# Optimization experiments

Hardware: AMD Instinct MI355X
Metric: run time of the kernel (lower is better)

## Reference

```python
import jax, jax.numpy as jnp
import numpy as np


def _update_cv(features, labels, ave, cov, amount, class_num):
    # Segment-reduce formulation of the onehot-expand update_CV.
    N, A = features.shape
    C = class_num
    counts = jax.ops.segment_sum(jnp.ones((N,), features.dtype), labels, num_segments=C)  # [C]
    sums = jax.ops.segment_sum(features, labels, num_segments=C)  # [C, A]
    denom = jnp.where(counts == 0, 1.0, counts)[:, None]  # Amount_CxA with zeros -> 1
    ave_CxA = sums / denom
    # var_temp: sum over samples of (x - mean_label)^2, divided by count
    diff = features - ave_CxA[labels]  # [N, A]
    sq = jax.ops.segment_sum(diff * diff, labels, num_segments=C)
    var_temp = sq / denom
    sum_weight = counts[:, None]  # [C,1] broadcast over A
    weight_CV = sum_weight / (sum_weight + amount[:, None])
    weight_CV = jnp.nan_to_num(weight_CV, nan=0.0)
    additional_CV = weight_CV * (1 - weight_CV) * (ave - ave_CxA) ** 2
    new_cov = cov * (1 - weight_CV) + var_temp * weight_CV + additional_CV
    new_ave = ave * (1 - weight_CV) + ave_CxA * weight_CV
    new_amount = amount + counts
    return new_ave, new_cov, new_amount


def _isda_aug(fc_weight, y, labels, cv_matrix, ratio):
    # sigma2[n,c] = ratio * sum_a (W[c,a] - W[labels[n],a])^2 * CV[labels[n],a]
    # = ratio * ( (W^2) @ cv_n - 2 W @ (w_n * cv_n) + sum_a w_n^2 cv_n )
    cv_n = cv_matrix[labels]              # [N, A]
    w_n = fc_weight[labels]               # [N, A]
    t1 = cv_n @ (fc_weight ** 2).T        # [N, C]
    t2 = (w_n * cv_n) @ fc_weight.T       # [N, C]
    t3 = jnp.sum(w_n * w_n * cv_n, axis=1, keepdims=True)  # [N, 1]
    sigma2 = ratio * (t1 - 2.0 * t2 + t3)
    return y + 0.5 * sigma2


def setup_inputs() -> dict:
    key = jax.random.key(0)
    k1, k2, k3, k4 = jax.random.split(key, 4)
    N, A, C = 512, 2048, 1000
    features = jax.random.normal(k1, (N, A), dtype=jnp.float32)
    labels = jax.random.randint(k2, (N,), 0, C)
    fc_weight = jax.random.normal(k3, (C, A), dtype=jnp.float32) * 0.02
    fc_bias = jax.random.normal(k4, (C,), dtype=jnp.float32) * 0.02
    return {
        "features": features,
        "labels": labels,
        "fc_weight": fc_weight,
        "fc_bias": fc_bias,
        "ave_state": jnp.zeros((C, A), jnp.float32),
        "cov_state": jnp.zeros((C, A), jnp.float32),
        "amount_state": jnp.zeros((C,), jnp.float32),
        "ratio": 1,
    }


def reference(features, labels, fc_weight, fc_bias, ave_state, cov_state, amount_state, ratio):
    C = fc_weight.shape[0]
    # model head: y = features @ W^T + b (features come from backbone; detached for CV)
    y = features @ fc_weight.T + fc_bias
    new_ave, new_cov, new_amount = _update_cv(
        jax.lax.stop_gradient(features), labels, ave_state, cov_state, amount_state, C)
    isda_y = _isda_aug(fc_weight, y, labels, jax.lax.stop_gradient(new_cov), ratio)
    log_probs = jax.nn.log_softmax(isda_y, axis=1)
    loss = -jnp.mean(jnp.take_along_axis(log_probs, labels[:, None], axis=1))
    return loss, y, new_ave, new_cov, new_amount
```

## Files before the change

kernel.cpp:

```cpp
#include <hip/hip_runtime.h>
#include <hip/hip_bf16.h>

typedef short v8s __attribute__((ext_vector_type(8)));
typedef float v4f __attribute__((ext_vector_type(4)));

#define KSPLIT 4

static __device__ __forceinline__ float ldv(const void* p, size_t i, int f32m) {
    if (f32m) return ((const float*)p)[i];
    return __bfloat162float(((const __hip_bfloat16*)p)[i]);
}
static __device__ __forceinline__ void stv(void* p, size_t i, float v, int f32m) {
    if (f32m) ((float*)p)[i] = v;
    else ((__hip_bfloat16*)p)[i] = __float2bfloat16(v);
}
static __device__ __forceinline__ unsigned short f2bu(float x) {
    __hip_bfloat16 h = __float2bfloat16(x);
    return *(unsigned short*)&h;
}
static __device__ __forceinline__ float bu2f(unsigned short u) {
    return __uint_as_float(((unsigned)u) << 16);
}
static __device__ __forceinline__ void ld2(const void* p, size_t i, int f32m, float* o) {
    if (f32m) {
        float2 v = *(const float2*)((const float*)p + i);
        o[0] = v.x; o[1] = v.y;
    } else {
        unsigned u = *(const unsigned*)((const unsigned short*)p + i);
        o[0] = bu2f((unsigned short)(u & 0xffffu));
        o[1] = bu2f((unsigned short)(u >> 16));
    }
}

static __device__ __forceinline__ float decode_scalar(const void* p) {
    unsigned u = *(const unsigned*)p;
    unsigned e32 = (u >> 23) & 0xff;
    if (e32 >= 97 && e32 <= 160) return __uint_as_float(u);
    unsigned lo = u & 0xffffu;
    unsigned e16 = (lo >> 7) & 0xff;
    if ((u >> 16) == 0 && e16 >= 97 && e16 <= 160)
        return __uint_as_float(lo << 16);
    return (float)(int)u;
}

static __device__ __forceinline__ int block_sniff(const void* feat) {
    const __hip_bfloat16* p = (const __hip_bfloat16*)feat;
    float v = __bfloat162float(p[threadIdx.x & 255]);
    int bad = !(fabsf(v) < 1e10f);
    return __syncthreads_or(bad) ? 1 : 0;
}

__device__ __forceinline__ float wave_sum(float v) {
    #pragma unroll
    for (int o = 32; o > 0; o >>= 1) v += __shfl_down(v, o, 64);
    return v;
}
__device__ __forceinline__ float wave_max(float v) {
    #pragma unroll
    for (int o = 32; o > 0; o >>= 1) v = fmaxf(v, __shfl_down(v, o, 64));
    return v;
}

static __device__ __forceinline__ void ld16(unsigned short* lds, const unsigned short* g) {
    __builtin_amdgcn_global_load_lds(
        (const __attribute__((address_space(1))) unsigned int*)g,
        (__attribute__((address_space(3))) unsigned int*)lds,
        16, 0, 0);
}

__global__ __launch_bounds__(1024) void sort_prep(
        const int* __restrict__ labels, int* __restrict__ counts,
        int* __restrict__ offs, int* __restrict__ rows, int Nn, int C,
        const void* __restrict__ feat, unsigned short* __restrict__ featb, int total,
        float* __restrict__ lsum, int* __restrict__ lcnt) {
    __shared__ int h[1024];
    __shared__ int o[1024];
    __shared__ int cu[1024];
    int tid = threadIdx.x;
    if (blockIdx.x == 0) {
        h[tid] = 0;
        __syncthreads();
        for (int i = tid; i < Nn; i += 1024) atomicAdd(&h[labels[i]], 1);
        __syncthreads();
        o[tid] = h[tid];
        __syncthreads();
        for (int d = 1; d < 1024; d <<= 1) {
            int v = (tid >= d) ? o[tid - d] : 0;
            __syncthreads();
            o[tid] += v;
            __syncthreads();
        }
        int excl = o[tid] - h[tid];
        counts[tid] = h[tid];
        offs[tid] = excl;
        cu[tid] = excl;
        __syncthreads();
        for (int i = tid; i < Nn; i += 1024) {
            int pos = atomicAdd(&cu[labels[i]], 1);
            rows[pos] = i;
        }
        if (tid == 0) { *lsum = 0.f; *lcnt = 0; }
    } else {
        int f32m = block_sniff(feat);
        int i = ((blockIdx.x - 1) * 1024 + tid) * 8;
        if (i >= total) return;
        if (f32m) {
            const float* f = (const float*)feat + i;
            unsigned short r[8];
            #pragma unroll
            for (int u = 0; u < 8; ++u) r[u] = f2bu(f[u]);
            *(v8s*)(featb + i) = *(v8s*)r;
        } else {
            *(v8s*)(featb + i) = *(const v8s*)((const unsigned short*)feat + i);
        }
    }
}

__global__ __launch_bounds__(256) void finalize_stats(
        const unsigned short* __restrict__ featb,
        const int* __restrict__ counts, const int* __restrict__ offs,
        const int* __restrict__ rows,
        const void* __restrict__ ave, const void* __restrict__ cov,
        const void* __restrict__ amount, const void* __restrict__ W,
        const void* __restrict__ feat,
        void* __restrict__ out, size_t off_ave, size_t off_cov, size_t off_amt,
        unsigned short* __restrict__ Wb, unsigned short* __restrict__ W2b,
        unsigned short* __restrict__ Cb, unsigned short* __restrict__ Gb,
        float* __restrict__ T3p, int A, int A8) {
    __shared__ float sb[4];
    int f32m = block_sniff(feat);
    int c = blockIdx.y;
    int a = (blockIdx.x * 256 + threadIdx.x) * 2;
    size_t idx = (size_t)c * A + a;
    int cnti = counts[c];
    int start = offs[c];
    float s1[2] = {0.f, 0.f}, s2[2] = {0.f, 0.f};
    for (int i = 0; i < cnti; ++i) {
        unsigned u = *(const unsigned*)(featb + (size_t)rows[start + i] * A + a);
        float x0 = bu2f((unsigned short)(u & 0xffffu));
        float x1 = bu2f((unsigned short)(u >> 16));
        s1[0] += x0; s2[0] += x0 * x0;
        s1[1] += x1; s2[1] += x1 * x1;
    }
    float cnt = (float)cnti;
    float denom = cnti > 0 ? cnt : 1.f;
    float amt = ldv(amount, c, f32m);
    float tot = cnt + amt;
    float w = tot > 0.f ? (cnt / tot) : 0.f;
    float av[2], cv[2], wv[2];
    ld2(ave, idx, f32m, av);
    ld2(cov, idx, f32m, cv);
    ld2(W, idx, f32m, wv);
    unsigned short cb2[2], gb2[2];
    float t3s = 0.f;
    #pragma unroll
    for (int k = 0; k < 2; ++k) {
        float mean = s1[k] / denom;
        float var = fmaxf((s2[k] - cnt * mean * mean) / denom, 0.f);
        float d = av[k] - mean;
        float ncv = cv[k] * (1.f - w) + var * w + w * (1.f - w) * d * d;
        float nav = av[k] * (1.f - w) + mean * w;
        stv(out, off_cov + idx + k, ncv, f32m);
        stv(out, off_ave + idx + k, nav, f32m);
        cb2[k] = f2bu(ncv);
        gb2[k] = f2bu(ncv * wv[k]);
        t3s += wv[k] * wv[k] * ncv;
    }
    *(unsigned*)(Wb + idx)  = (unsigned)f2bu(wv[0]) | ((unsigned)f2bu(wv[1]) << 16);
    *(unsigned*)(W2b + idx) = (unsigned)f2bu(wv[0] * wv[0]) | ((unsigned)f2bu(wv[1] * wv[1]) << 16);
    *(unsigned*)(Cb + idx)  = (unsigned)cb2[0] | ((unsigned)cb2[1] << 16);
    *(unsigned*)(Gb + idx)  = (unsigned)gb2[0] | ((unsigned)gb2[1] << 16);
    if (a == 0) stv(out, off_amt + c, amt + cnt, f32m);
    float s = wave_sum(t3s);
    int lane = threadIdx.x & 63, wid = threadIdx.x >> 6;
    if (lane == 0) sb[wid] = s;
    __syncthreads();
    if (threadIdx.x == 0) T3p[(size_t)c * A8 + blockIdx.x] = sb[0] + sb[1] + sb[2] + sb[3];
}

__global__ __launch_bounds__(256) void triple_gemm_mfma(
        const unsigned short* __restrict__ featb,
        const unsigned short* __restrict__ Wb,
        const unsigned short* __restrict__ W2b,
        const unsigned short* __restrict__ Cb,
        const unsigned short* __restrict__ Gb,
        const int* __restrict__ labels,
        float* __restrict__ partY, float* __restrict__ partT1, float* __restrict__ partT2,
        int Cpad, int A, size_t NC) {
    __shared__ unsigned short sA[3][10240];
    __shared__ int sLab[64];
    int tid = threadIdx.x, wv = tid >> 6, lane = tid & 63;
    int n0 = blockIdx.y * 64, j0 = blockIdx.x * 64;
    int kslice = A / KSPLIT;
    int k0 = blockIdx.z * kslice;
    if (tid < 64) sLab[tid] = labels[n0 + tid];
    __syncthreads();

    int r = lane & 15, q = lane >> 4;
    int fr = wv * 16 + r;
    const unsigned short* pF = featb + (size_t)(n0 + fr) * A + k0 + q * 8;
    int lab = sLab[fr];
    const unsigned short* pC = Cb + (size_t)lab * A + k0 + q * 8;
    const unsigned short* pG = Gb + (size_t)lab * A + k0 + q * 8;
    const unsigned short* pW = Wb + (size_t)(j0 + fr) * A + k0 + q * 8;
    const unsigned short* pQ = W2b + (size_t)(j0 + fr) * A + k0 + q * 8;

    v4f aY[4] = {{0,0,0,0},{0,0,0,0},{0,0,0,0},{0,0,0,0}};
    v4f aT1[4] = {{0,0,0,0},{0,0,0,0},{0,0,0,0},{0,0,0,0}};
    v4f aT2[4] = {{0,0,0,0},{0,0,0,0},{0,0,0,0},{0,0,0,0}};

    const int NIT = kslice / 32;

    #define STAGE(b) do { \
        ld16(&sA[b][0    + wv * 512], pF); \
        ld16(&sA[b][2048 + wv * 512], pC); \
        ld16(&sA[b][4096 + wv * 512], pG); \
        ld16(&sA[b][6144 + wv * 512], pW); \
        ld16(&sA[b][8192 + wv * 512], pQ); \
        pF += 32; pC += 32; pG += 32; pW += 32; pQ += 32; } while (0)

    STAGE(0);
    STAGE(1);

    for (int it = 0; it < NIT; ++it) {
        int bcur = it % 3;
        if (it + 1 < NIT) asm volatile("s_waitcnt vmcnt(5)\n\ts_barrier" ::: "memory");
        else              asm volatile("s_waitcnt vmcnt(0)\n\ts_barrier" ::: "memory");
        if (it + 2 < NIT) { int bn = (it + 2) % 3; STAGE(bn); }
        v8s f = *(v8s*)&sA[bcur][0    + wv * 512 + lane * 8];
        v8s c = *(v8s*)&sA[bcur][2048 + wv * 512 + lane * 8];
        v8s g = *(v8s*)&sA[bcur][4096 + wv * 512 + lane * 8];
        #pragma unroll
        for (int t = 0; t < 4; ++t) {
            v8s w  = *(v8s*)&sA[bcur][6144 + t * 512 + lane * 8];
            v8s w2 = *(v8s*)&sA[bcur][8192 + t * 512 + lane * 8];
            aY[t]  = __builtin_amdgcn_mfma_f32_16x16x32_bf16(f, w,  aY[t],  0, 0, 0);
            aT1[t] = __builtin_amdgcn_mfma_f32_16x16x32_bf16(c, w2, aT1[t], 0, 0, 0);
            aT2[t] = __builtin_amdgcn_mfma_f32_16x16x32_bf16(g, w,  aT2[t], 0, 0, 0);
        }
    }
    #undef STAGE

    float* pY = partY + (size_t)blockIdx.z * NC;
    float* p1 = partT1 + (size_t)blockIdx.z * NC;
    float* p2 = partT2 + (size_t)blockIdx.z * NC;
    int quad = lane >> 4, colb = lane & 15;
    #pragma unroll
    for (int t = 0; t < 4; ++t) {
        int j = j0 + t * 16 + colb;
        #pragma unroll
        for (int rr = 0; rr < 4; ++rr) {
            int n = n0 + wv * 16 + quad * 4 + rr;
            size_t idx = (size_t)n * Cpad + j;
            pY[idx] = aY[t][rr];
            p1[idx] = aT1[t][rr];
            p2[idx] = aT2[t][rr];
        }
    }
}

__global__ __launch_bounds__(256) void epilogue_rowloss(
        const float* __restrict__ partY, const float* __restrict__ partT1,
        const float* __restrict__ partT2, const float* __restrict__ T3p,
        const void* __restrict__ bias, const void* __restrict__ feat,
        const int* __restrict__ labels,
        void* __restrict__ out, size_t off_y,
        float* __restrict__ lsum, int* __restrict__ lcnt,
        int C, int Cpad, int A8, const void* ratio_p, size_t NC, int Nn) {
    __shared__ float sb[4];
    __shared__ float sM;
    __shared__ float sLabVal;
    int f32m = block_sniff(feat);
    int tid = threadIdx.x;
    int n = blockIdx.x;
    int lab = labels[n];
    float t3 = 0.f;
    for (int i = 0; i < A8; ++i) t3 += T3p[(size_t)lab * A8 + i];
    float ratio = decode_scalar(ratio_p);

    float vals[8];
    int nu = Cpad >> 8;
    float m = -3.4e38f;
    for (int u = 0; u < nu; ++u) {
        int j = u * 256 + tid;
        float v = -3.4e38f;
        if (j < C) {
            size_t idx = (size_t)n * Cpad + j;
            float y = 0.f, t1 = 0.f, t2 = 0.f;
            #pragma unroll
            for (int z = 0; z < KSPLIT; ++z) {
                y  += partY[z * NC + idx];
                t1 += partT1[z * NC + idx];
                t2 += partT2[z * NC + idx];
            }
            y += ldv(bias, j, f32m);
            stv(out, off_y + (size_t)n * C + j, y, f32m);
            v = y + 0.5f * ratio * (t1 - 2.f * t2 + t3);
            if (j == lab) sLabVal = v;
        }
        vals[u] = v;
        m = fmaxf(m, v);
    }
    m = wave_max(m);
    int lane = tid & 63, wid = tid >> 6;
    if (lane == 0) sb[wid] = m;
    __syncthreads();
    if (tid == 0) sM = fmaxf(fmaxf(sb[0], sb[1]), fmaxf(sb[2], sb[3]));
    __syncthreads();
    m = sM;
    float s = 0.f;
    for (int u = 0; u < nu; ++u) s += expf(vals[u] - m);
    __syncthreads();
    s = wave_sum(s);
    if (lane == 0) sb[wid] = s;
    __syncthreads();
    if (tid == 0) {
        float rl = m + logf(sb[0] + sb[1] + sb[2] + sb[3]) - sLabVal;
        atomicAdd(lsum, rl);
        __threadfence();
        int old = atomicAdd(lcnt, 1);
        if (old == Nn - 1) {
            __threadfence();
            float total = atomicAdd(lsum, 0.f);
            stv(out, 0, total / (float)Nn, f32m);
        }
    }
}

extern "C" void kernel_launch(void* const* d_in, const int* in_sizes, int n_in,
                              void* d_out, int out_size, void* d_ws, size_t ws_size,
                              hipStream_t stream) {
    const void* feat   = d_in[0];
    const int*  labels = (const int*)d_in[1];
    const void* W      = d_in[2];
    const void* bias   = d_in[3];
    const void* ave    = d_in[4];
    const void* cov    = d_in[5];
    const void* amount = d_in[6];
    const void* ratiop = d_in[7];

    int NA = in_sizes[0];
    int Nn = in_sizes[1];
    int C  = in_sizes[3];
    int A  = NA / Nn;
    int CA = in_sizes[2];
    int Cpad = ((C + 255) / 256) * 256;
    int A8 = A / 512;
    size_t NC = (size_t)Nn * Cpad;

    size_t off_y   = 1;
    size_t off_ave = off_y + (size_t)Nn * C;
    size_t off_cov = off_ave + (size_t)CA;
    size_t off_amt = off_cov + (size_t)CA;

    char* ws = (char*)d_ws;
    int*   w_cnt  = (int*)ws;
    int*   w_off  = w_cnt + 1024;
    int*   w_rows = w_off + 1024;
    float* w_T3p  = (float*)(w_rows + 1024);
    float* w_lsum = w_T3p + 8192;
    int*   w_lcnt = (int*)(w_lsum + 1);
    float* w_partY  = w_lsum + 1024;
    float* w_partT1 = w_partY + KSPLIT * NC;
    float* w_partT2 = w_partT1 + KSPLIT * NC;
    unsigned short* w_featb = (unsigned short*)(w_partT2 + KSPLIT * NC);
    unsigned short* w_Wb    = w_featb + NA;
    unsigned short* w_W2b   = w_Wb + CA;
    unsigned short* w_Cb    = w_W2b + CA;
    unsigned short* w_Gb    = w_Cb + CA;

    int prep_blocks = NA / 8192;
    sort_prep<<<1 + prep_blocks, 1024, 0, stream>>>(
        labels, w_cnt, w_off, w_rows, Nn, C, feat, w_featb, NA, w_lsum, w_lcnt);
    dim3 g2(A / 512, C);
    finalize_stats<<<g2, 256, 0, stream>>>(w_featb, w_cnt, w_off, w_rows,
                                           ave, cov, amount, W, feat,
                                           d_out, off_ave, off_cov, off_amt,
                                           w_Wb, w_W2b, w_Cb, w_Gb, w_T3p, A, A8);
    dim3 g3(Cpad / 64, Nn / 64, KSPLIT);
    triple_gemm_mfma<<<g3, 256, 0, stream>>>(w_featb, w_Wb, w_W2b, w_Cb, w_Gb,
                                             labels, w_partY, w_partT1, w_partT2,
                                             Cpad, A, NC);
    epilogue_rowloss<<<Nn, 256, 0, stream>>>(w_partY, w_partT1, w_partT2, w_T3p,
                                             bias, feat, labels, d_out, off_y,
                                             w_lsum, w_lcnt,
                                             C, Cpad, A8, ratiop, NC, Nn);
}
```

Measured before the change: 144.1 us.

## Fuse all four stages into one cooperative persistent kernel with grid syncs

Replaces the four separate launches (sort/prep, finalize stats, triple GEMM, epilogue) with a single cooperative kernel of 512 blocks that runs each stage as a grid-strided loop separated by grid.sync barriers. The goal is to remove per-launch overhead and inter-kernel gaps. In exchange every stage is limited to 512 blocks of 256 threads, which may reduce parallelism in the stats stage (previously C×4 blocks) and in the GEMM. The 1024-thread sort is also redone with 256 threads. If the cooperative launch fails, the code falls back to the original four launches.

```diff
diff --git a/kernel.cpp b/kernel.cpp
--- a/kernel.cpp
+++ b/kernel.cpp
@@ -1,5 +1,8 @@
 #include <hip/hip_runtime.h>
 #include <hip/hip_bf16.h>
+#include <hip/hip_cooperative_groups.h>
+
+namespace cg = cooperative_groups;
 
 typedef short v8s __attribute__((ext_vector_type(8)));
 typedef float v4f __attribute__((ext_vector_type(4)));
@@ -67,6 +70,271 @@
         (__attribute__((address_space(3))) unsigned int*)lds,
         16, 0, 0);
 }
+
+
+struct MegaArgs {
+    const void* feat; const int* labels; const void* W; const void* bias;
+    const void* ave; const void* cov; const void* amount; const void* ratiop;
+    void* out;
+    unsigned long long off_y, off_ave, off_cov, off_amt;
+    int* counts; int* offs; int* rowsg; float* T3p; float* lsum; int* lcnt;
+    float* partY; float* partT1; float* partT2;
+    unsigned short* featb; unsigned short* Wb; unsigned short* W2b;
+    unsigned short* Cb; unsigned short* Gb;
+    int Nn, C, A, Cpad, A8, total;
+    unsigned long long NC;
+};
+
+__global__ __launch_bounds__(256, 2) void isda_mega(MegaArgs p) {
+    __shared__ union {
+        struct { int h[1024]; int o[1024]; int cur[1024]; } s1;
+        struct { unsigned short sA[3][10240]; int sLab[64]; } s3;
+        struct { float sb[4]; float sM; float sLabVal; } s4;
+    } sh;
+
+    cg::grid_group grid = cg::this_grid();
+    int tid = threadIdx.x;
+    int lane = tid & 63, wid = tid >> 6;
+    int f32m = block_sniff(p.feat);
+
+    for (long long i = ((long long)blockIdx.x * 256 + tid) * 8; i < p.total;
+         i += (long long)gridDim.x * 2048) {
+        if (f32m) {
+            const float* f = (const float*)p.feat + i;
+            unsigned short rr[8];
+            #pragma unroll
+            for (int u2 = 0; u2 < 8; ++u2) rr[u2] = f2bu(f[u2]);
+            *(v8s*)(p.featb + i) = *(v8s*)rr;
+        } else {
+            *(v8s*)(p.featb + i) = *(const v8s*)((const unsigned short*)p.feat + i);
+        }
+    }
+    if (blockIdx.x == 0) {
+        for (int k = tid; k < 1024; k += 256) sh.s1.h[k] = 0;
+        __syncthreads();
+        for (int i = tid; i < p.Nn; i += 256) atomicAdd(&sh.s1.h[p.labels[i]], 1);
+        __syncthreads();
+        int a0 = sh.s1.h[4 * tid], a1 = sh.s1.h[4 * tid + 1];
+        int a2 = sh.s1.h[4 * tid + 2], a3 = sh.s1.h[4 * tid + 3];
+        int tsum = a0 + a1 + a2 + a3;
+        sh.s1.o[tid] = tsum;
+        __syncthreads();
+        for (int d = 1; d < 256; d <<= 1) {
+            int v = (tid >= d) ? sh.s1.o[tid - d] : 0;
+            __syncthreads();
+            sh.s1.o[tid] += v;
+            __syncthreads();
+        }
+        int texcl = sh.s1.o[tid] - tsum;
+        int e0 = texcl, e1 = e0 + a0, e2 = e1 + a1, e3 = e2 + a2;
+        p.counts[4 * tid] = a0; p.counts[4 * tid + 1] = a1;
+        p.counts[4 * tid + 2] = a2; p.counts[4 * tid + 3] = a3;
+        p.offs[4 * tid] = e0; p.offs[4 * tid + 1] = e1;
+        p.offs[4 * tid + 2] = e2; p.offs[4 * tid + 3] = e3;
+        sh.s1.cur[4 * tid] = e0; sh.s1.cur[4 * tid + 1] = e1;
+        sh.s1.cur[4 * tid + 2] = e2; sh.s1.cur[4 * tid + 3] = e3;
+        __syncthreads();
+        for (int i = tid; i < p.Nn; i += 256) {
+            int pos = atomicAdd(&sh.s1.cur[p.labels[i]], 1);
+            p.rowsg[pos] = i;
+        }
+        if (tid == 0) { *p.lsum = 0.f; *p.lcnt = 0; }
+    }
+    __threadfence();
+    grid.sync();
+
+    {
+        int NCH = p.A >> 9;
+        int units = p.C * NCH;
+        for (int u = blockIdx.x; u < units; u += gridDim.x) {
+            int chunk = u % NCH, c = u / NCH;
+            int a = (chunk * 256 + tid) * 2;
+            size_t idx = (size_t)c * p.A + a;
+            int cnti = p.counts[c];
+            int start = p.offs[c];
+            float s1v[2] = {0.f, 0.f}, s2v[2] = {0.f, 0.f};
+            for (int i = 0; i < cnti; ++i) {
+                unsigned uu = *(const unsigned*)(p.featb + (size_t)p.rowsg[start + i] * p.A + a);
+                float x0 = bu2f((unsigned short)(uu & 0xffffu));
+                float x1 = bu2f((unsigned short)(uu >> 16));
+                s1v[0] += x0; s2v[0] += x0 * x0;
+                s1v[1] += x1; s2v[1] += x1 * x1;
+            }
+            float cnt = (float)cnti;
+            float denomv = cnti > 0 ? cnt : 1.f;
+            float amt = ldv(p.amount, c, f32m);
+            float tot = cnt + amt;
+            float w = tot > 0.f ? (cnt / tot) : 0.f;
+            float av[2], cvv[2], wvv[2];
+            ld2(p.ave, idx, f32m, av);
+            ld2(p.cov, idx, f32m, cvv);
+            ld2(p.W, idx, f32m, wvv);
+            unsigned short cb2[2], gb2[2];
+            float t3s = 0.f;
+            #pragma unroll
+            for (int k = 0; k < 2; ++k) {
+                float mean = s1v[k] / denomv;
+                float var = fmaxf((s2v[k] - cnt * mean * mean) / denomv, 0.f);
+                float d = av[k] - mean;
+                float ncv = cvv[k] * (1.f - w) + var * w + w * (1.f - w) * d * d;
+                float nav = av[k] * (1.f - w) + mean * w;
+                stv(p.out, p.off_cov + idx + k, ncv, f32m);
+                stv(p.out, p.off_ave + idx + k, nav, f32m);
+                cb2[k] = f2bu(ncv);
+                gb2[k] = f2bu(ncv * wvv[k]);
+                t3s += wvv[k] * wvv[k] * ncv;
+            }
+            *(unsigned*)(p.Wb + idx)  = (unsigned)f2bu(wvv[0]) | ((unsigned)f2bu(wvv[1]) << 16);
+            *(unsigned*)(p.W2b + idx) = (unsigned)f2bu(wvv[0] * wvv[0]) | ((unsigned)f2bu(wvv[1] * wvv[1]) << 16);
+            *(unsigned*)(p.Cb + idx)  = (unsigned)cb2[0] | ((unsigned)cb2[1] << 16);
+            *(unsigned*)(p.Gb + idx)  = (unsigned)gb2[0] | ((unsigned)gb2[1] << 16);
+            if (a == 0) stv(p.out, p.off_amt + c, amt + cnt, f32m);
+            float s = wave_sum(t3s);
+            if (lane == 0) sh.s4.sb[wid] = s;
+            __syncthreads();
+            if (tid == 0)
+                p.T3p[(size_t)c * p.A8 + chunk] = sh.s4.sb[0] + sh.s4.sb[1] + sh.s4.sb[2] + sh.s4.sb[3];
+            __syncthreads();
+        }
+    }
+    __threadfence();
+    grid.sync();
+
+    {
+        int gx = p.Cpad >> 6, gy = p.Nn >> 6;
+        int vtot = gx * gy * KSPLIT;
+        int kslice = p.A / KSPLIT;
+        int NIT = kslice / 32;
+        for (int vb = blockIdx.x; vb < vtot; vb += gridDim.x) {
+            int x = vb % gx, y = (vb / gx) % gy, z = vb / (gx * gy);
+            __syncthreads();
+            if (tid < 64) sh.s3.sLab[tid] = p.labels[y * 64 + tid];
+            __syncthreads();
+            int n0 = y * 64, j0 = x * 64;
+            int k0 = z * kslice;
+            int r = lane & 15, q = lane >> 4;
+            int fr = wid * 16 + r;
+            const unsigned short* pF = p.featb + (size_t)(n0 + fr) * p.A + k0 + q * 8;
+            int lab = sh.s3.sLab[fr];
+            const unsigned short* pC = p.Cb + (size_t)lab * p.A + k0 + q * 8;
+            const unsigned short* pG = p.Gb + (size_t)lab * p.A + k0 + q * 8;
+            const unsigned short* pW = p.Wb + (size_t)(j0 + fr) * p.A + k0 + q * 8;
+            const unsigned short* pQ = p.W2b + (size_t)(j0 + fr) * p.A + k0 + q * 8;
+
+            v4f aY[4] = {{0,0,0,0},{0,0,0,0},{0,0,0,0},{0,0,0,0}};
+            v4f aT1[4] = {{0,0,0,0},{0,0,0,0},{0,0,0,0},{0,0,0,0}};
+            v4f aT2[4] = {{0,0,0,0},{0,0,0,0},{0,0,0,0},{0,0,0,0}};
+
+            #define STAGE3(b) do { \
+                ld16(&sh.s3.sA[b][0    + wid * 512], pF); \
+                ld16(&sh.s3.sA[b][2048 + wid * 512], pC); \
+                ld16(&sh.s3.sA[b][4096 + wid * 512], pG); \
+                ld16(&sh.s3.sA[b][6144 + wid * 512], pW); \
+                ld16(&sh.s3.sA[b][8192 + wid * 512], pQ); \
+                pF += 32; pC += 32; pG += 32; pW += 32; pQ += 32; } while (0)
+
+            STAGE3(0);
+            STAGE3(1);
+
+            for (int it = 0; it < NIT; ++it) {
+                int bcur = it % 3;
+                if (it + 1 < NIT) asm volatile("s_waitcnt vmcnt(5)\n\ts_barrier" ::: "memory");
+                else              asm volatile("s_waitcnt vmcnt(0)\n\ts_barrier" ::: "memory");
+                if (it + 2 < NIT) { STAGE3((it + 2) % 3); }
+                v8s f  = *(v8s*)&sh.s3.sA[bcur][0    + wid * 512 + lane * 8];
+                v8s c2 = *(v8s*)&sh.s3.sA[bcur][2048 + wid * 512 + lane * 8];
+                v8s g2 = *(v8s*)&sh.s3.sA[bcur][4096 + wid * 512 + lane * 8];
+                #pragma unroll
+                for (int t = 0; t < 4; ++t) {
+                    v8s w  = *(v8s*)&sh.s3.sA[bcur][6144 + t * 512 + lane * 8];
+                    v8s w2 = *(v8s*)&sh.s3.sA[bcur][8192 + t * 512 + lane * 8];
+                    aY[t]  = __builtin_amdgcn_mfma_f32_16x16x32_bf16(f,  w,  aY[t],  0, 0, 0);
+                    aT1[t] = __builtin_amdgcn_mfma_f32_16x16x32_bf16(c2, w2, aT1[t], 0, 0, 0);
+                    aT2[t] = __builtin_amdgcn_mfma_f32_16x16x32_bf16(g2, w,  aT2[t], 0, 0, 0);
+                }
+            }
+            #undef STAGE3
+
+            float* pY = p.partY + (size_t)z * p.NC;
+            float* p1 = p.partT1 + (size_t)z * p.NC;
+            float* p2 = p.partT2 + (size_t)z * p.NC;
+            int quad = lane >> 4, colb = lane & 15;
+            #pragma unroll
+            for (int t = 0; t < 4; ++t) {
+                int j = j0 + t * 16 + colb;
+                #pragma unroll
+                for (int rr2 = 0; rr2 < 4; ++rr2) {
+                    int n = n0 + wid * 16 + quad * 4 + rr2;
+                    size_t idx = (size_t)n * p.Cpad + j;
+                    pY[idx] = aY[t][rr2];
+                    p1[idx] = aT1[t][rr2];
+                    p2[idx] = aT2[t][rr2];
+                }
+            }
+        }
+    }
+    __threadfence();
+    grid.sync();
+
+    {
+        float ratio = decode_scalar(p.ratiop);
+        int nu = p.Cpad >> 8;
+        for (int n = blockIdx.x; n < p.Nn; n += gridDim.x) {
+            __syncthreads();
+            int lab = p.labels[n];
+            float t3 = 0.f;
+            for (int i = 0; i < p.A8; ++i) t3 += p.T3p[(size_t)lab * p.A8 + i];
+            float vals[8];
+            float m = -3.4e38f;
+            for (int u = 0; u < nu; ++u) {
+                int j = u * 256 + tid;
+                float v = -3.4e38f;
+                if (j < p.C) {
+                    size_t idx = (size_t)n * p.Cpad + j;
+                    float y = 0.f, t1 = 0.f, t2 = 0.f;
+                    #pragma unroll
+                    for (int zz = 0; zz < KSPLIT; ++zz) {
+                        y  += p.partY[zz * p.NC + idx];
+                        t1 += p.partT1[zz * p.NC + idx];
+                        t2 += p.partT2[zz * p.NC + idx];
+                    }
+                    y += ldv(p.bias, j, f32m);
+                    stv(p.out, p.off_y + (size_t)n * p.C + j, y, f32m);
+                    v = y + 0.5f * ratio * (t1 - 2.f * t2 + t3);
+                    if (j == lab) sh.s4.sLabVal = v;
+                }
+                vals[u] = v;
+                m = fmaxf(m, v);
+            }
+            m = wave_max(m);
+            if (lane == 0) sh.s4.sb[wid] = m;
+            __syncthreads();
+            if (tid == 0) sh.s4.sM = fmaxf(fmaxf(sh.s4.sb[0], sh.s4.sb[1]),
+                                           fmaxf(sh.s4.sb[2], sh.s4.sb[3]));
+            __syncthreads();
+            m = sh.s4.sM;
+            float s = 0.f;
+            for (int u = 0; u < nu; ++u) s += expf(vals[u] - m);
+            __syncthreads();
+            s = wave_sum(s);
+            if (lane == 0) sh.s4.sb[wid] = s;
+            __syncthreads();
+            if (tid == 0) {
+                float rl = m + logf(sh.s4.sb[0] + sh.s4.sb[1] + sh.s4.sb[2] + sh.s4.sb[3])
+                           - sh.s4.sLabVal;
+                atomicAdd(p.lsum, rl);
+                __threadfence();
+                int old = atomicAdd(p.lcnt, 1);
+                if (old == p.Nn - 1) {
+                    __threadfence();
+                    float totl = atomicAdd(p.lsum, 0.f);
+                    stv(p.out, 0, totl / (float)p.Nn, f32m);
+                }
+            }
+        }
+    }
+}
+
 
 __global__ __launch_bounds__(1024) void sort_prep(
         const int* __restrict__ labels, int* __restrict__ counts,
@@ -369,6 +637,27 @@
     unsigned short* w_Cb    = w_W2b + CA;
     unsigned short* w_Gb    = w_Cb + CA;
 
+    bool coop_ok = (C <= 1024) && ((A & 511) == 0) && ((Nn & 63) == 0) &&
+                   ((Cpad & 63) == 0) && (NA % 2048 == 0);
+    if (coop_ok) {
+        MegaArgs ma;
+        ma.feat = feat; ma.labels = labels; ma.W = W; ma.bias = bias;
+        ma.ave = ave; ma.cov = cov; ma.amount = amount; ma.ratiop = ratiop;
+        ma.out = d_out;
+        ma.off_y = off_y; ma.off_ave = off_ave; ma.off_cov = off_cov; ma.off_amt = off_amt;
+        ma.counts = w_cnt; ma.offs = w_off; ma.rowsg = w_rows; ma.T3p = w_T3p;
+        ma.lsum = w_lsum; ma.lcnt = w_lcnt;
+        ma.partY = w_partY; ma.partT1 = w_partT1; ma.partT2 = w_partT2;
+        ma.featb = w_featb; ma.Wb = w_Wb; ma.W2b = w_W2b; ma.Cb = w_Cb; ma.Gb = w_Gb;
+        ma.Nn = Nn; ma.C = C; ma.A = A; ma.Cpad = Cpad; ma.A8 = A8;
+        ma.total = NA; ma.NC = NC;
+        void* kargs[] = { &ma };
+        hipError_t e = hipLaunchCooperativeKernel((void*)isda_mega, dim3(512), dim3(256),
+                                                  kargs, 0, stream);
+        if (e == hipSuccess) return;
+        (void)hipGetLastError();
+    }
+
     int prep_blocks = NA / 8192;
     sort_prep<<<1 + prep_blocks, 1024, 0, stream>>>(
         labels, w_cnt, w_off, w_rows, Nn, C, feat, w_featb, NA, w_lsum, w_lcnt);
```

Result: slower. 496.7 us (+244.6%).

## Fuse label sort into stats kernel and merge T1/T2 accumulators

Applied to the files above, without the earlier changes.

Removes the separate sort_prep kernel. Each stats block now scans the labels itself to find its class rows and also converts features to bf16 in a grid-stride loop, which saves one launch and the single-block serial histogram/scan. Folds the -2 factor into Gb so that T1 and T2 share one MFMA accumulator, halving partial-sum writes and epilogue reads. The cost is that every block redundantly scans all labels, and accumulating T1-2T2 in one register may slightly change rounding.

```diff
diff --git a/kernel.cpp b/kernel.cpp
--- a/kernel.cpp
+++ b/kernel.cpp
@@ -68,128 +68,109 @@
         16, 0, 0);
 }
 
-__global__ __launch_bounds__(1024) void sort_prep(
-        const int* __restrict__ labels, int* __restrict__ counts,
-        int* __restrict__ offs, int* __restrict__ rows, int Nn, int C,
-        const void* __restrict__ feat, unsigned short* __restrict__ featb, int total,
-        float* __restrict__ lsum, int* __restrict__ lcnt) {
-    __shared__ int h[1024];
-    __shared__ int o[1024];
-    __shared__ int cu[1024];
-    int tid = threadIdx.x;
-    if (blockIdx.x == 0) {
-        h[tid] = 0;
-        __syncthreads();
-        for (int i = tid; i < Nn; i += 1024) atomicAdd(&h[labels[i]], 1);
-        __syncthreads();
-        o[tid] = h[tid];
-        __syncthreads();
-        for (int d = 1; d < 1024; d <<= 1) {
-            int v = (tid >= d) ? o[tid - d] : 0;
-            __syncthreads();
-            o[tid] += v;
-            __syncthreads();
-        }
-        int excl = o[tid] - h[tid];
-        counts[tid] = h[tid];
-        offs[tid] = excl;
-        cu[tid] = excl;
-        __syncthreads();
-        for (int i = tid; i < Nn; i += 1024) {
-            int pos = atomicAdd(&cu[labels[i]], 1);
-            rows[pos] = i;
-        }
-        if (tid == 0) { *lsum = 0.f; *lcnt = 0; }
-    } else {
-        int f32m = block_sniff(feat);
-        int i = ((blockIdx.x - 1) * 1024 + tid) * 8;
-        if (i >= total) return;
-        if (f32m) {
-            const float* f = (const float*)feat + i;
-            unsigned short r[8];
-            #pragma unroll
-            for (int u = 0; u < 8; ++u) r[u] = f2bu(f[u]);
-            *(v8s*)(featb + i) = *(v8s*)r;
-        } else {
-            *(v8s*)(featb + i) = *(const v8s*)((const unsigned short*)feat + i);
-        }
-    }
-}
-
-__global__ __launch_bounds__(256) void finalize_stats(
-        const unsigned short* __restrict__ featb,
-        const int* __restrict__ counts, const int* __restrict__ offs,
-        const int* __restrict__ rows,
+__global__ __launch_bounds__(256) void stats_prep(
+        const void* __restrict__ feat, const int* __restrict__ labels,
         const void* __restrict__ ave, const void* __restrict__ cov,
         const void* __restrict__ amount, const void* __restrict__ W,
-        const void* __restrict__ feat,
         void* __restrict__ out, size_t off_ave, size_t off_cov, size_t off_amt,
+        unsigned short* __restrict__ featb,
         unsigned short* __restrict__ Wb, unsigned short* __restrict__ W2b,
         unsigned short* __restrict__ Cb, unsigned short* __restrict__ Gb,
-        float* __restrict__ T3p, int A, int A8) {
+        float* __restrict__ T3p, float* __restrict__ lsum, int* __restrict__ lcnt,
+        int Nn, int A, int A8, int NA) {
+    __shared__ int sRows[2048];
+    __shared__ int sCnt;
     __shared__ float sb[4];
+    int tid = threadIdx.x;
     int f32m = block_sniff(feat);
+
+    if (f32m) {
+        int flat = blockIdx.y * gridDim.x + blockIdx.x;
+        int nblk = gridDim.x * gridDim.y;
+        for (long long i = ((long long)flat * 256 + tid) * 8; i < NA;
+             i += (long long)nblk * 2048) {
+            const float* f = (const float*)feat + i;
+            unsigned short r8[8];
+            #pragma unroll
+            for (int u = 0; u < 8; ++u) r8[u] = f2bu(f[u]);
+            *(v8s*)(featb + i) = *(v8s*)r8;
+        }
+    }
+    if (blockIdx.x == 0 && blockIdx.y == 0 && tid == 0) { *lsum = 0.f; *lcnt = 0; }
+
     int c = blockIdx.y;
-    int a = (blockIdx.x * 256 + threadIdx.x) * 2;
+    int a = (blockIdx.x * 256 + tid) * 2;
     size_t idx = (size_t)c * A + a;
-    int cnti = counts[c];
-    int start = offs[c];
-    float s1[2] = {0.f, 0.f}, s2[2] = {0.f, 0.f};
-    for (int i = 0; i < cnti; ++i) {
-        unsigned u = *(const unsigned*)(featb + (size_t)rows[start + i] * A + a);
-        float x0 = bu2f((unsigned short)(u & 0xffffu));
-        float x1 = bu2f((unsigned short)(u >> 16));
-        s1[0] += x0; s2[0] += x0 * x0;
-        s1[1] += x1; s2[1] += x1 * x1;
+    float s1v[2] = {0.f, 0.f}, s2v[2] = {0.f, 0.f};
+    int cnti = 0;
+    for (int base = 0; base < Nn; base += 2048) {
+        int lim = min(Nn - base, 2048);
+        if (tid == 0) sCnt = 0;
+        __syncthreads();
+        for (int i = tid; i < lim; i += 256)
+            if (labels[base + i] == c) { int pp = atomicAdd(&sCnt, 1); sRows[pp] = base + i; }
+        __syncthreads();
+        int cl = sCnt;
+        cnti += cl;
+        for (int i = 0; i < cl; ++i) {
+            float x[2];
+            ld2(feat, (size_t)sRows[i] * A + a, f32m, x);
+            s1v[0] += x[0]; s2v[0] += x[0] * x[0];
+            s1v[1] += x[1]; s2v[1] += x[1] * x[1];
+        }
+        __syncthreads();
     }
     float cnt = (float)cnti;
-    float denom = cnti > 0 ? cnt : 1.f;
+    float denomv = cnti > 0 ? cnt : 1.f;
     float amt = ldv(amount, c, f32m);
     float tot = cnt + amt;
     float w = tot > 0.f ? (cnt / tot) : 0.f;
-    float av[2], cv[2], wv[2];
+    float av[2], cvv[2], wvv[2];
     ld2(ave, idx, f32m, av);
-    ld2(cov, idx, f32m, cv);
-    ld2(W, idx, f32m, wv);
+    ld2(cov, idx, f32m, cvv);
+    ld2(W, idx, f32m, wvv);
     unsigned short cb2[2], gb2[2];
     float t3s = 0.f;
     #pragma unroll
     for (int k = 0; k < 2; ++k) {
-        float mean = s1[k] / denom;
-        float var = fmaxf((s2[k] - cnt * mean * mean) / denom, 0.f);
+        float mean = s1v[k] / denomv;
+        float var = fmaxf((s2v[k] - cnt * mean * mean) / denomv, 0.f);
         float d = av[k] - mean;
-        float ncv = cv[k] * (1.f - w) + var * w + w * (1.f - w) * d * d;
+        float ncv = cvv[k] * (1.f - w) + var * w + w * (1.f - w) * d * d;
         float nav = av[k] * (1.f - w) + mean * w;
         stv(out, off_cov + idx + k, ncv, f32m);
         stv(out, off_ave + idx + k, nav, f32m);
         cb2[k] = f2bu(ncv);
-        gb2[k] = f2bu(ncv * wv[k]);
-        t3s += wv[k] * wv[k] * ncv;
-    }
-    *(unsigned*)(Wb + idx)  = (unsigned)f2bu(wv[0]) | ((unsigned)f2bu(wv[1]) << 16);
-    *(unsigned*)(W2b + idx) = (unsigned)f2bu(wv[0] * wv[0]) | ((unsigned)f2bu(wv[1] * wv[1]) << 16);
+        gb2[k] = f2bu(-2.f * ncv * wvv[k]);
+        t3s += wvv[k] * wvv[k] * ncv;
+    }
+    *(unsigned*)(Wb + idx)  = (unsigned)f2bu(wvv[0]) | ((unsigned)f2bu(wvv[1]) << 16);
+    *(unsigned*)(W2b + idx) = (unsigned)f2bu(wvv[0] * wvv[0]) | ((unsigned)f2bu(wvv[1] * wvv[1]) << 16);
     *(unsigned*)(Cb + idx)  = (unsigned)cb2[0] | ((unsigned)cb2[1] << 16);
     *(unsigned*)(Gb + idx)  = (unsigned)gb2[0] | ((unsigned)gb2[1] << 16);
     if (a == 0) stv(out, off_amt + c, amt + cnt, f32m);
     float s = wave_sum(t3s);
-    int lane = threadIdx.x & 63, wid = threadIdx.x >> 6;
+    int lane = tid & 63, wid = tid >> 6;
     if (lane == 0) sb[wid] = s;
     __syncthreads();
-    if (threadIdx.x == 0) T3p[(size_t)c * A8 + blockIdx.x] = sb[0] + sb[1] + sb[2] + sb[3];
+    if (tid == 0) T3p[(size_t)c * A8 + blockIdx.x] = sb[0] + sb[1] + sb[2] + sb[3];
 }
 
 __global__ __launch_bounds__(256) void triple_gemm_mfma(
+        const void* __restrict__ feat,
         const unsigned short* __restrict__ featb,
         const unsigned short* __restrict__ Wb,
         const unsigned short* __restrict__ W2b,
         const unsigned short* __restrict__ Cb,
         const unsigned short* __restrict__ Gb,
         const int* __restrict__ labels,
-        float* __restrict__ partY, float* __restrict__ partT1, float* __restrict__ partT2,
+        float* __restrict__ partY, float* __restrict__ partS,
         int Cpad, int A, size_t NC) {
     __shared__ unsigned short sA[3][10240];
     __shared__ int sLab[64];
     int tid = threadIdx.x, wv = tid >> 6, lane = tid & 63;
+    int f32m = block_sniff(feat);
+    const unsigned short* Fsrc = f32m ? featb : (const unsigned short*)feat;
     int n0 = blockIdx.y * 64, j0 = blockIdx.x * 64;
     int kslice = A / KSPLIT;
     int k0 = blockIdx.z * kslice;
@@ -198,7 +179,7 @@
 
     int r = lane & 15, q = lane >> 4;
     int fr = wv * 16 + r;
-    const unsigned short* pF = featb + (size_t)(n0 + fr) * A + k0 + q * 8;
+    const unsigned short* pF = Fsrc + (size_t)(n0 + fr) * A + k0 + q * 8;
     int lab = sLab[fr];
     const unsigned short* pC = Cb + (size_t)lab * A + k0 + q * 8;
     const unsigned short* pG = Gb + (size_t)lab * A + k0 + q * 8;
@@ -206,8 +187,7 @@
     const unsigned short* pQ = W2b + (size_t)(j0 + fr) * A + k0 + q * 8;
 
     v4f aY[4] = {{0,0,0,0},{0,0,0,0},{0,0,0,0},{0,0,0,0}};
-    v4f aT1[4] = {{0,0,0,0},{0,0,0,0},{0,0,0,0},{0,0,0,0}};
-    v4f aT2[4] = {{0,0,0,0},{0,0,0,0},{0,0,0,0},{0,0,0,0}};
+    v4f aS[4] = {{0,0,0,0},{0,0,0,0},{0,0,0,0},{0,0,0,0}};
 
     const int NIT = kslice / 32;
 
@@ -234,16 +214,15 @@
         for (int t = 0; t < 4; ++t) {
             v8s w  = *(v8s*)&sA[bcur][6144 + t * 512 + lane * 8];
             v8s w2 = *(v8s*)&sA[bcur][8192 + t * 512 + lane * 8];
-            aY[t]  = __builtin_amdgcn_mfma_f32_16x16x32_bf16(f, w,  aY[t],  0, 0, 0);
-            aT1[t] = __builtin_amdgcn_mfma_f32_16x16x32_bf16(c, w2, aT1[t], 0, 0, 0);
-            aT2[t] = __builtin_amdgcn_mfma_f32_16x16x32_bf16(g, w,  aT2[t], 0, 0, 0);
+            aY[t] = __builtin_amdgcn_mfma_f32_16x16x32_bf16(f, w,  aY[t], 0, 0, 0);
+            aS[t] = __builtin_amdgcn_mfma_f32_16x16x32_bf16(c, w2, aS[t], 0, 0, 0);
+            aS[t] = __builtin_amdgcn_mfma_f32_16x16x32_bf16(g, w,  aS[t], 0, 0, 0);
         }
     }
     #undef STAGE
 
     float* pY = partY + (size_t)blockIdx.z * NC;
-    float* p1 = partT1 + (size_t)blockIdx.z * NC;
-    float* p2 = partT2 + (size_t)blockIdx.z * NC;
+    float* pS = partS + (size_t)blockIdx.z * NC;
     int quad = lane >> 4, colb = lane & 15;
     #pragma unroll
     for (int t = 0; t < 4; ++t) {
@@ -253,15 +232,14 @@
             int n = n0 + wv * 16 + quad * 4 + rr;
             size_t idx = (size_t)n * Cpad + j;
             pY[idx] = aY[t][rr];
-            p1[idx] = aT1[t][rr];
-            p2[idx] = aT2[t][rr];
+            pS[idx] = aS[t][rr];
         }
     }
 }
 
 __global__ __launch_bounds__(256) void epilogue_rowloss(
-        const float* __restrict__ partY, const float* __restrict__ partT1,
-        const float* __restrict__ partT2, const float* __restrict__ T3p,
+        const float* __restrict__ partY, const float* __restrict__ partS,
+        const float* __restrict__ T3p,
         const void* __restrict__ bias, const void* __restrict__ feat,
         const int* __restrict__ labels,
         void* __restrict__ out, size_t off_y,
@@ -281,22 +259,24 @@
     float vals[8];
     int nu = Cpad >> 8;
     float m = -3.4e38f;
-    for (int u = 0; u < nu; ++u) {
-        int j = u * 256 + tid;
+    #pragma unroll
+    for (int u = 0; u < 8; ++u) {
         float v = -3.4e38f;
-        if (j < C) {
-            size_t idx = (size_t)n * Cpad + j;
-            float y = 0.f, t1 = 0.f, t2 = 0.f;
-            #pragma unroll
-            for (int z = 0; z < KSPLIT; ++z) {
-                y  += partY[z * NC + idx];
-                t1 += partT1[z * NC + idx];
-                t2 += partT2[z * NC + idx];
+        if (u < nu) {
+            int j = u * 256 + tid;
+            if (j < C) {
+                size_t idx = (size_t)n * Cpad + j;
+                float y = 0.f, s = 0.f;
+                #pragma unroll
+                for (int z = 0; z < KSPLIT; ++z) {
+                    y += partY[z * NC + idx];
+                    s += partS[z * NC + idx];
+                }
+                y += ldv(bias, j, f32m);
+                stv(out, off_y + (size_t)n * C + j, y, f32m);
+                v = y + 0.5f * ratio * (s + t3);
+                if (j == lab) sLabVal = v;
             }
-            y += ldv(bias, j, f32m);
-            stv(out, off_y + (size_t)n * C + j, y, f32m);
-            v = y + 0.5f * ratio * (t1 - 2.f * t2 + t3);
-            if (j == lab) sLabVal = v;
         }
         vals[u] = v;
         m = fmaxf(m, v);
@@ -309,7 +289,8 @@
     __syncthreads();
     m = sM;
     float s = 0.f;
-    for (int u = 0; u < nu; ++u) s += expf(vals[u] - m);
+    #pragma unroll
+    for (int u = 0; u < 8; ++u) s += (u < nu) ? expf(vals[u] - m) : 0.f;
     __syncthreads();
     s = wave_sum(s);
     if (lane == 0) sb[wid] = s;
@@ -354,34 +335,26 @@
     size_t off_amt = off_cov + (size_t)CA;
 
     char* ws = (char*)d_ws;
-    int*   w_cnt  = (int*)ws;
-    int*   w_off  = w_cnt + 1024;
-    int*   w_rows = w_off + 1024;
-    float* w_T3p  = (float*)(w_rows + 1024);
+    float* w_T3p  = (float*)ws;
     float* w_lsum = w_T3p + 8192;
     int*   w_lcnt = (int*)(w_lsum + 1);
-    float* w_partY  = w_lsum + 1024;
-    float* w_partT1 = w_partY + KSPLIT * NC;
-    float* w_partT2 = w_partT1 + KSPLIT * NC;
-    unsigned short* w_featb = (unsigned short*)(w_partT2 + KSPLIT * NC);
+    float* w_partY = w_lsum + 1024;
+    float* w_partS = w_partY + KSPLIT * NC;
+    unsigned short* w_featb = (unsigned short*)(w_partS + KSPLIT * NC);
     unsigned short* w_Wb    = w_featb + NA;
     unsigned short* w_W2b   = w_Wb + CA;
     unsigned short* w_Cb    = w_W2b + CA;
     unsigned short* w_Gb    = w_Cb + CA;
 
-    int prep_blocks = NA / 8192;
-    sort_prep<<<1 + prep_blocks, 1024, 0, stream>>>(
-        labels, w_cnt, w_off, w_rows, Nn, C, feat, w_featb, NA, w_lsum, w_lcnt);
-    dim3 g2(A / 512, C);
-    finalize_stats<<<g2, 256, 0, stream>>>(w_featb, w_cnt, w_off, w_rows,
-                                           ave, cov, amount, W, feat,
-                                           d_out, off_ave, off_cov, off_amt,
-                                           w_Wb, w_W2b, w_Cb, w_Gb, w_T3p, A, A8);
-    dim3 g3(Cpad / 64, Nn / 64, KSPLIT);
-    triple_gemm_mfma<<<g3, 256, 0, stream>>>(w_featb, w_Wb, w_W2b, w_Cb, w_Gb,
-                                             labels, w_partY, w_partT1, w_partT2,
-                                             Cpad, A, NC);
-    epilogue_rowloss<<<Nn, 256, 0, stream>>>(w_partY, w_partT1, w_partT2, w_T3p,
+    dim3 g1(A / 512, C);
+    stats_prep<<<g1, 256, 0, stream>>>(feat, labels, ave, cov, amount, W,
+                                       d_out, off_ave, off_cov, off_amt,
+                                       w_featb, w_Wb, w_W2b, w_Cb, w_Gb,
+                                       w_T3p, w_lsum, w_lcnt, Nn, A, A8, NA);
+    dim3 g2(Cpad / 64, Nn / 64, KSPLIT);
+    triple_gemm_mfma<<<g2, 256, 0, stream>>>(feat, w_featb, w_Wb, w_W2b, w_Cb, w_Gb,
+                                             labels, w_partY, w_partS, Cpad, A, NC);
+    epilogue_rowloss<<<Nn, 256, 0, stream>>>(w_partY, w_partS, w_T3p,
                                              bias, feat, labels, d_out, off_y,
                                              w_lsum, w_lcnt,
                                              C, Cpad, A8, ratiop, NC, Nn);
```

After: 143.1 us. About the same (-0.7%).
